# Performance work log

Hardware: AMD Instinct MI355X
Metric: run time of the kernel (lower is better)

## Reference

```python
import jax, jax.numpy as jnp
import numpy as np

# S4D (diagonal state space) layer, version=1, bidirectional.
# Faithful to the standard minimal S4D: ZOH-discretized diagonal kernel via
# Vandermonde, causal FFT convolution, D skip, GELU, then 1x1-conv GLU.


def _s4d(u, log_dt, C_re, C_im, log_A_real, A_imag, D_skip, W_glu, b_glu):
    # u: (B, L, H)
    B, L, Hd = u.shape
    dt = jnp.exp(log_dt)                                   # (H,)
    A = -jnp.exp(log_A_real) + 1j * A_imag                 # (H, N2) complex
    dtA = A * dt[:, None]                                  # (H, N2)
    C = (C_re + 1j * C_im) * (jnp.exp(dtA) - 1.0) / A      # (H, N2)
    V = jnp.exp(dtA[:, :, None] * jnp.arange(L))           # (H, N2, L) Vandermonde
    K = 2.0 * jnp.einsum('hn,hnl->hl', C, V).real          # (H, L) SSM kernel
    uT = jnp.swapaxes(u, 1, 2)                             # (B, H, L)
    n = 2 * L                                              # zero-pad for causal conv
    y = jnp.fft.irfft(jnp.fft.rfft(uT, n=n) * jnp.fft.rfft(K, n=n), n=n)[..., :L]
    y = y + uT * D_skip[:, None]                           # skip connection
    y = jax.nn.gelu(y, approximate=False)                  # torch nn.GELU (exact erf)
    # output_linear: Conv1d(H, 2H, 1) + GLU(dim=-2)
    z = jnp.einsum('oh,bhl->bol', W_glu, y) + b_glu[None, :, None]
    y = z[:, :Hd] * jax.nn.sigmoid(z[:, Hd:])
    return jnp.swapaxes(y, 1, 2)                           # (B, L, H)


def setup_inputs() -> dict:
    key = jax.random.key(0)
    B, L, D, N = 64, 2048, 256, 64
    N2 = N // 2
    kx, kf, kr = jax.random.split(key, 3)

    def make_params(k0):
        ks = jax.random.split(k0, 6)
        log_dt = jax.random.uniform(ks[0], (D,)) * (np.log(0.1) - np.log(0.001)) + np.log(0.001)
        C_re = jax.random.normal(ks[1], (D, N2))
        C_im = jax.random.normal(ks[2], (D, N2))
        log_A_real = jnp.log(0.5 * jnp.ones((D, N2), dtype=jnp.float32))
        A_imag = np.pi * jnp.broadcast_to(jnp.arange(N2, dtype=jnp.float32), (D, N2))
        D_skip = jax.random.normal(ks[3], (D,))
        W_glu = jax.random.normal(ks[4], (2 * D, D)) / np.sqrt(D)
        b_glu = jax.random.normal(ks[5], (2 * D,)) * 0.01
        return log_dt, C_re, C_im, log_A_real, A_imag, D_skip, W_glu, b_glu

    pf = make_params(kf)
    pr = make_params(kr)
    names = ['log_dt', 'C_re', 'C_im', 'log_A_real', 'A_imag', 'D_skip', 'W_glu', 'b_glu']
    inp = {'x': jax.random.normal(kx, (B, L, D), dtype=jnp.float32)}
    for n_, v in zip(names, pf):
        inp[n_] = v
    for n_, v in zip(names, pr):
        inp[n_ + '_rev'] = v
    return inp


def reference(x, log_dt, C_re, C_im, log_A_real, A_imag, D_skip, W_glu, b_glu,
              log_dt_rev, C_re_rev, C_im_rev, log_A_real_rev, A_imag_rev,
              D_skip_rev, W_glu_rev, b_glu_rev):
    y_fwd = _s4d(x, log_dt, C_re, C_im, log_A_real, A_imag, D_skip, W_glu, b_glu)
    y_rev = _s4d(x[:, ::-1], log_dt_rev, C_re_rev, C_im_rev, log_A_real_rev,
                 A_imag_rev, D_skip_rev, W_glu_rev, b_glu_rev)
    return y_fwd + y_rev[:, ::-1]
```

## Files before the change

### kernel.cpp

```cpp
#include <hip/hip_runtime.h>
#include <hip/hip_bf16.h>
#include <math.h>

#define Bb 64
#define Ll 2048
#define Hh 256
#define N2v 32
#define NCH 4
#define CLEN (Ll / NCH)

#define WF_OFF 1024
#define BF_OFF 525312
#define GOLD_OFF 529408
#define A2_OFF 529408
#define AF_OFF 4723712
#define WT_OFF 13112320
#define XT_OFF 13243392
#define S_OFF  80352256
#define GT_OFF 214569984
#define WS_NEED 348787712ull
#define GNEW_OFF XT_OFF

typedef __hip_bfloat16 bf16;
typedef __bf16 bf16x8 __attribute__((ext_vector_type(8)));
typedef float f32x4 __attribute__((ext_vector_type(4)));
typedef _Float16 f16;
typedef _Float16 f16x2 __attribute__((ext_vector_type(2)));
typedef _Float16 f16x4 __attribute__((ext_vector_type(4)));
typedef _Float16 f16x8 __attribute__((ext_vector_type(8)));

__device__ __forceinline__ float b2f(bf16 v) { return __bfloat162float(v); }
__device__ __forceinline__ float ldf(const float* p, int i) { return p[i]; }
__device__ __forceinline__ float ldf(const bf16* p, int i) { return b2f(p[i]); }

__device__ __forceinline__ void gl2lds16(const void* g, void* l) {
  __builtin_amdgcn_global_load_lds((const __attribute__((address_space(1))) void*)g,
                                   (__attribute__((address_space(3))) void*)l, 16, 0, 0);
}

__device__ __forceinline__ f32x4 mfma16(f16x8 a, f16x8 b, f32x4 c) {
  return __builtin_amdgcn_mfma_f32_16x16x32_f16(a, b, c, 0, 0, 0);
}

__device__ __forceinline__ bool input_is_bf16(const void* logA) {
  unsigned u = *(const unsigned*)logA;
  return (u >> 16) == (u & 0xffffu);
}

__global__ void s4d_prep(const void* Wf, const void* bfb, const void* Wr,
                         const void* brb, const void* logA, char* ws) {
  const bool bf = input_is_bf16(logA);
  bf16* wdst = (bf16*)(ws + WF_OFF);
  float* bdst = (float*)(ws + BF_OFF);
  const int i = blockIdx.x * 256 + threadIdx.x;
  if (i < 262144) {
    const int dstR = i >> 8, k = i & 255;
    const int ht = dstR >> 7, c = dstR & 127;
    const int mat = c >> 5, hl = c & 31;
    const int srow = mat * 256 + ht * 32 + hl;
    const void* src = (srow < 512) ? Wf : Wr;
    const int j = ((srow < 512) ? srow : srow - 512) * 256 + k;
    const float v = bf ? b2f(((const bf16*)src)[j]) : ((const float*)src)[j];
    wdst[i] = __float2bfloat16(v);
  } else if (i < 262144 + 1024) {
    const int j = i - 262144;
    const void* src = (j < 512) ? bfb : brb;
    const int k = (j < 512) ? j : j - 512;
    bdst[j] = bf ? b2f(((const bf16*)src)[k]) : ((const float*)src)[k];
  }
}

struct ScanP {
  const void* x;
  const void* prm[2][6];
  char* ws;
};

__global__ __launch_bounds__(64) void s4d_prepA(ScanP p) {
  const int d = blockIdx.x >> 8, h = blockIdx.x & 255;
  const int lane = threadIdx.x;
  __shared__ float Ksh[64];
  char* ws = p.ws;
  const bool bf = input_is_bf16(p.prm[0][3]);
#define LDP(w_, i_) (bf ? b2f(((const bf16*)p.prm[d][w_])[i_]) : ((const float*)p.prm[d][w_])[i_])
  const float dt = expf(LDP(0, h));
  const float dsk = LDP(5, h);
  float Kv = 0.f;
  const float dl = (float)lane;
  for (int n = 0; n < 32; ++n) {
    const int idx = h * 32 + n;
    const float Ar = -expf(LDP(3, idx));
    const float Ai = LDP(4, idx);
    const float th = Ai * dt, rr = Ar * dt;
    const float er = expf(rr);
    const float wr = er * cosf(th), wi = er * sinf(th);
    const float den = 1.f / (Ar * Ar + Ai * Ai);
    const float Er = wr - 1.f, Ei = wi;
    const float qr = (Er * Ar + Ei * Ai) * den, qi = (Ei * Ar - Er * Ai) * den;
    const float CR = LDP(1, idx), CI = LDP(2, idx);
    const float cre = 2.f * (CR * qr - CI * qi), cim = 2.f * (CR * qi + CI * qr);
    const float pe = expf(rr * dl), pang = th * dl;
    Kv += cre * pe * cosf(pang) - cim * pe * sinf(pang);
  }
  Ksh[lane] = Kv;
  if (lane < 32) {
    const int idx = h * 32 + lane;
    const float Ar = -expf(LDP(3, idx));
    const float Ai = LDP(4, idx);
    const float th = Ai * dt, rr = Ar * dt;
    const float e64 = expf(rr * 64.f);
    float2 wt;
    wt.x = e64 * cosf(th * 64.f);
    wt.y = e64 * sinf(th * 64.f);
    ((float2*)(ws + WT_OFF))[(d * 256 + h) * 32 + lane] = wt;
  }
  __syncthreads();
  f16* arow = (f16*)(ws + AF_OFF) + ((size_t)(d * 256 + h) * 64 + lane) * 128;
  for (int j = 0; j < 64; ++j) {
    float v = 0.f;
    if (d == 0) { if (j <= lane) v = Ksh[lane - j]; }
    else        { if (j >= lane) v = Ksh[j - lane]; }
    if (j == lane) v += dsk;
    arow[j] = (f16)v;
  }
  const float pexp = (d == 0) ? (float)(lane + 1) : (float)(64 - lane);
  for (int n = 0; n < 32; ++n) {
    const int idx = h * 32 + n;
    const float Ar = -expf(LDP(3, idx));
    const float Ai = LDP(4, idx);
    const float th = Ai * dt, rr = Ar * dt;
    const float er = expf(rr);
    const float wr = er * cosf(th), wi = er * sinf(th);
    const float den = 1.f / (Ar * Ar + Ai * Ai);
    const float Er = wr - 1.f, Ei = wi;
    const float qr = (Er * Ar + Ei * Ai) * den, qi = (Ei * Ar - Er * Ai) * den;
    const float CR = LDP(1, idx), CI = LDP(2, idx);
    const float cre = 2.f * (CR * qr - CI * qi), cim = 2.f * (CR * qi + CI * qr);
    const float pe = expf(rr * pexp), pang = th * pexp;
    const float pwr = pe * cosf(pang), pwi = pe * sinf(pang);
    arow[64 + 2 * n]     = (f16)(cre * pwr - cim * pwi);
    arow[64 + 2 * n + 1] = (f16)(-(cre * pwi + cim * pwr));
  }
  {
    const int n = lane >> 1, im = lane & 1;
    const int idx = h * 32 + n;
    const float Ar = -expf(LDP(3, idx));
    const float Ai = LDP(4, idx);
    const float th = Ai * dt, rr = Ar * dt;
    f16* a2 = (f16*)(ws + A2_OFF) + ((size_t)h * 128 + d * 64 + lane) * 64;
    for (int i = 0; i < 64; ++i) {
      const float pp = (d == 0) ? (float)(63 - i) : (float)i;
      const float e = expf(rr * pp), ang = th * pp;
      a2[i] = (f16)(im ? e * sinf(ang) : e * cosf(ang));
    }
  }
#undef LDP
}

template <typename T>
__device__ __forceinline__ void t1_body(const T* __restrict__ x, char* ws) {
  __shared__ f16 tile[8][264];
  const int b = blockIdx.x, h0 = blockIdx.y * 8;
  const int t = threadIdx.x;
  f16* xT = (f16*)(ws + XT_OFF);
  const int hh = t & 7, lo = t >> 3;
  const int wh = t >> 5, q = t & 31;
  for (int l0 = 0; l0 < 2048; l0 += 256) {
    __syncthreads();
#pragma unroll
    for (int ps = 0; ps < 8; ++ps) {
      const int l = l0 + ps * 32 + lo;
      tile[hh][ps * 32 + lo] = (f16)ldf(x, (b * 2048 + l) * 256 + h0 + hh);
    }
    __syncthreads();
    f16x8 v = *(const f16x8*)(&tile[wh][q * 8]);
    *(f16x8*)(xT + ((size_t)(h0 + wh) * 64 + b) * 2048 + l0 + q * 8) = v;
  }
}

__global__ __launch_bounds__(256) void s4d_t1(const void* x, const void* logA, char* ws) {
  if (input_is_bf16(logA)) t1_body<bf16>((const bf16*)x, ws);
  else                     t1_body<float>((const float*)x, ws);
}

__global__ __launch_bounds__(256) void s4d_krs(char* __restrict__ ws) {
  __shared__ char lds[34816];
  const int bid = blockIdx.x;
  const int h = bid >> 4, cb = bid & 15;
  const int t = threadIdx.x, lane = t & 63, wave = t >> 6;
  const int lm = lane & 15, lq = lane >> 4;
  const f16* xT = (const f16*)(ws + XT_OFF);
  const char* a2b = ws + A2_OFF + (size_t)h * 128 * 64 * 2;
  const int srow = lane >> 3;
  const int sch = (lane & 7) ^ srow;
#pragma unroll
  for (int j = 0; j < 4; ++j) {
    const int rb = wave * 4 + j;
    const int r = rb * 8 + srow;
    gl2lds16(a2b + r * 128 + sch * 16, lds + rb * 1024);
    const int col = cb * 128 + r;
    const int b_ = col >> 5, c_ = col & 31;
    gl2lds16((const char*)(xT + ((size_t)(h * 64 + b_) * 2048 + c_ * 64)) + sch * 16,
             lds + 16384 + rb * 1024);
  }
  __syncthreads();
  f32x4 acc[2][8];
#pragma unroll
  for (int i = 0; i < 2; ++i)
#pragma unroll
    for (int j = 0; j < 8; ++j) acc[i][j] = (f32x4){0.f, 0.f, 0.f, 0.f};
#pragma unroll
  for (int kb = 0; kb < 2; ++kb) {
    const int cA = kb * 4 + lq;
    f16x8 au[2], a2f[8];
#pragma unroll
    for (int i = 0; i < 2; ++i) {
      const int r = wave * 32 + i * 16 + lm;
      au[i] = *(const f16x8*)(lds + 16384 + r * 128 + ((cA ^ (r & 7)) * 16));
    }
#pragma unroll
    for (int j = 0; j < 8; ++j) {
      const int r = j * 16 + lm;
      a2f[j] = *(const f16x8*)(lds + r * 128 + ((cA ^ (r & 7)) * 16));
    }
#pragma unroll
    for (int i = 0; i < 2; ++i)
#pragma unroll
      for (int j = 0; j < 8; ++j) acc[i][j] = mfma16(au[i], a2f[j], acc[i][j]);
  }
  __syncthreads();
  f16* Cl = (f16*)lds;
#pragma unroll
  for (int i = 0; i < 2; ++i)
#pragma unroll
    for (int j = 0; j < 8; ++j)
#pragma unroll
      for (int r = 0; r < 4; ++r)
        Cl[(wave * 32 + i * 16 + lq * 4 + r) * 136 + j * 16 + lm] = (f16)acc[i][j][r];
  __syncthreads();
  const int n = t & 31, dir = (t >> 5) & 1, bl = wave;
  const float2 wt = ((const float2*)(ws + WT_OFF))[(dir * 256 + h) * 32 + n];
  f16* Sg = (f16*)(ws + S_OFF) + ((size_t)h * 2048 + cb * 128 + bl * 32) * 128 + dir * 64 + 2 * n;
  const f16* Cr = Cl + (size_t)(bl * 32) * 136 + dir * 64 + 2 * n;
  float sr = 0.f, si = 0.f;
  const int c0 = dir ? 31 : 0, cstep = dir ? -1 : 1;
  for (int it = 0; it < 32; ++it) {
    const int c = c0 + it * cstep;
    f16x2 sv; sv[0] = (f16)sr; sv[1] = (f16)si;
    *(f16x2*)(Sg + (size_t)c * 128) = sv;
    const float rr = (float)Cr[c * 136], ri = (float)Cr[c * 136 + 1];
    const float a = sr;
    sr = wt.x * a - wt.y * si + rr;
    si = wt.x * si + wt.y * a + ri;
  }
}

__global__ __launch_bounds__(256) void s4d_k3(char* __restrict__ ws) {
  __shared__ char lds[57344];
  const int bid = blockIdx.x;
  const int h = bid >> 5, cb = bid & 31;
  const int t = threadIdx.x, lane = t & 63, wave = t >> 6;
  const int lm = lane & 15, lq = lane >> 4;
  const f16* xT = (const f16*)(ws + XT_OFF);
  const char* afb = ws + AF_OFF + (size_t)h * 64 * 128 * 2;
  const char* arb = ws + AF_OFF + (size_t)(256 + h) * 64 * 128 * 2;
  const char* sb = ws + S_OFF;
  {
    const int sr4 = lane >> 4, c16 = lane & 15;
#pragma unroll
    for (int j = 0; j < 4; ++j) {
      const int rb = wave * 4 + j;
      const int r = rb * 4 + sr4;
      const int sc = c16 ^ (r & 7);
      gl2lds16(afb + r * 256 + sc * 16, lds + rb * 1024);
      gl2lds16(arb + r * 256 + sc * 16, lds + 16384 + rb * 1024);
    }
  }
  {
    const int sr8 = lane >> 3, c8 = lane & 7;
#pragma unroll
    for (int j = 0; j < 2; ++j) {
      const int rb = wave * 2 + j;
      const int clr = rb * 8 + sr8;
      const int col = cb * 64 + clr;
      const int b_ = col >> 5, c_ = col & 31;
      const int sc = c8 ^ (clr & 7);
      gl2lds16((const char*)(xT + ((size_t)(h * 64 + b_) * 2048 + c_ * 64)) + sc * 16,
               lds + 32768 + rb * 1024);
      const char* srow = sb + ((size_t)h * 2048 + col) * 256;
      gl2lds16(srow + sc * 16,       lds + 40960 + rb * 1024);
      gl2lds16(srow + 128 + sc * 16, lds + 49152 + rb * 1024);
    }
  }
  __syncthreads();
  const int dir = wave >> 1, chf = wave & 1;
  const char* At = lds + dir * 16384;
  f32x4 acc[4][2];
#pragma unroll
  for (int i = 0; i < 4; ++i)
#pragma unroll
    for (int j = 0; j < 2; ++j) acc[i][j] = (f32x4){0.f, 0.f, 0.f, 0.f};
#pragma unroll
  for (int kb = 0; kb < 4; ++kb) {
    f16x8 av[4], bv[2];
    const int cA = kb * 4 + lq;
#pragma unroll
    for (int i = 0; i < 4; ++i) {
      const int r = i * 16 + lm;
      av[i] = *(const f16x8*)(At + r * 256 + ((cA ^ (r & 7)) * 16));
    }
    const char* Bt = lds + 32768 + ((kb < 2) ? 0 : (dir ? 16384 : 8192));
    const int cB = (kb & 1) * 4 + lq;
#pragma unroll
    for (int j = 0; j < 2; ++j) {
      const int r = chf * 32 + j * 16 + lm;
      bv[j] = *(const f16x8*)(Bt + r * 128 + ((cB ^ (r & 7)) * 16));
    }
#pragma unroll
    for (int i = 0; i < 4; ++i)
#pragma unroll
      for (int j = 0; j < 2; ++j) acc[i][j] = mfma16(av[i], bv[j], acc[i][j]);
  }
  f16* gT = (f16*)(ws + GT_OFF);
#pragma unroll
  for (int i = 0; i < 4; ++i)
#pragma unroll
    for (int j = 0; j < 2; ++j) {
      const int col = cb * 64 + chf * 32 + j * 16 + lm;
      const int b_ = col >> 5, c_ = col & 31;
      const int i0 = i * 16 + lq * 4;
      f16x4 o;
#pragma unroll
      for (int r = 0; r < 4; ++r) {
        const float y = acc[i][j][r];
        o[r] = (f16)(0.5f * y * (1.f + erff(y * 0.70710678118654752f)));
      }
      *(f16x4*)(gT + ((size_t)((dir * 256 + h) * 64 + b_)) * 2048 + c_ * 64 + i0) = o;
    }
}

__global__ __launch_bounds__(256) void s4d_tr(char* __restrict__ ws) {
  const int bid = blockIdx.x;
  const int mt = bid & 7, hq = (bid >> 3) & 7, b = (bid >> 6) & 63, dir = bid >> 12;
  const int lane = threadIdx.x & 63, wave = threadIdx.x >> 6;
  const int hb = hq * 32 + wave * 8;
  const f16* gT = (const f16*)(ws + GT_OFF);
  bf16* gm = (bf16*)(ws + GNEW_OFF) + (size_t)dir * (Bb * Ll * Hh);
#pragma unroll
  for (int mp = 0; mp < 4; ++mp) {
    const size_t l = (size_t)mt * 256 + mp * 64 + lane;
    ushort us[8];
#pragma unroll
    for (int e = 0; e < 8; ++e) {
      const float f = (float)gT[((size_t)((dir * 256 + hb + e) * 64 + b)) * 2048 + l];
      bf16 bb = __float2bfloat16(f);
      us[e] = *(ushort*)&bb;
    }
    uint4 o;
    o.x = (unsigned)us[0] | ((unsigned)us[1] << 16);
    o.y = (unsigned)us[2] | ((unsigned)us[3] << 16);
    o.z = (unsigned)us[4] | ((unsigned)us[5] << 16);
    o.w = (unsigned)us[6] | ((unsigned)us[7] << 16);
    *(uint4*)((char*)gm + ((size_t)b * 2048 + l) * 512 + hb * 2) = o;
  }
}

template <typename T>
__device__ __forceinline__ void scan_body(
    const T* __restrict__ x, const T* ldt_p, const T* cre_p, const T* cim_p,
    const T* lar_p, const T* aim_p, const T* dsk_p, bf16* gbase, float2* S) {
  const int t = threadIdx.x;
  const int lane = t & 63;
  const int ch = t >> 6;
  const int hloc = lane & 7;
  const int ngrp = lane >> 3;
  const int b = blockIdx.x;
  const int hblk = blockIdx.y;
  const int dir = blockIdx.z;
  const int h = hblk * 8 + hloc;

  const float dt = expf(ldf(ldt_p, h));
  float wre[4], wim[4], cre[4], cim[4], sre[4], sim[4];
#pragma unroll
  for (int j = 0; j < 4; ++j) {
    const int idx = h * N2v + ngrp * 4 + j;
    const float Ar = -expf(ldf(lar_p, idx));
    const float Ai = ldf(aim_p, idx);
    const float er = expf(Ar * dt);
    const float wr = er * cosf(Ai * dt), wi = er * sinf(Ai * dt);
    wre[j] = wr; wim[j] = wi;
    const float Er = wr - 1.0f, Ei = wi;
    const float den = 1.0f / (Ar * Ar + Ai * Ai);
    const float qr = (Er * Ar + Ei * Ai) * den;
    const float qi = (Ei * Ar - Er * Ai) * den;
    const float CR = ldf(cre_p, idx);
    const float CI = ldf(cim_p, idx);
    cre[j] = 2.0f * (CR * qr - CI * qi);
    cim[j] = 2.0f * (CR * qi + CI * qr);
    sre[j] = 0.0f; sim[j] = 0.0f;
  }
  const float dsk = ldf(dsk_p, h);

  const int base = b * (Ll * Hh) + h;
  const int stride = dir ? -Hh : Hh;
  const T* x0 = x + base + (dir ? (Ll - 1) * Hh : 0);
  bf16* g0 = gbase + dir * (Bb * Ll * Hh) + base + (dir ? (Ll - 1) * Hh : 0);

  if (ch < NCH - 1) {
    const T* xp = x0 + ch * CLEN * stride;
    for (int it = 0; it < CLEN / 4; ++it) {
      const float u0 = ldf(xp, 0);
      const float u1 = ldf(xp, stride);
      const float u2 = ldf(xp, 2 * stride);
      const float u3 = ldf(xp, 3 * stride);
      xp += 4 * stride;
#pragma unroll
      for (int k = 0; k < 4; ++k) {
        const float U = (k == 0) ? u0 : (k == 1) ? u1 : (k == 2) ? u2 : u3;
#pragma unroll
        for (int j = 0; j < 4; ++j) {
          const float a = sre[j], bb = sim[j];
          sre[j] = fmaf(wre[j], a, fmaf(-wim[j], bb, U));
          sim[j] = fmaf(wre[j], bb, wim[j] * a);
        }
      }
    }
#pragma unroll
    for (int j = 0; j < 4; ++j)
      S[((ch * 8 + ngrp) * 4 + j) * 8 + hloc] = (float2){sre[j], sim[j]};
  }
  __syncthreads();

  float pr[4], pi[4];
#pragma unroll
  for (int j = 0; j < 4; ++j) { pr[j] = wre[j]; pi[j] = wim[j]; }
  for (int q = 0; q < 9; ++q) {
#pragma unroll
    for (int j = 0; j < 4; ++j) {
      const float a = pr[j], bb = pi[j];
      pr[j] = fmaf(a, a, -bb * bb);
      pi[j] = 2.0f * a * bb;
    }
  }
#pragma unroll
  for (int j = 0; j < 4; ++j) { sre[j] = 0.0f; sim[j] = 0.0f; }
  for (int cc = 0; cc < ch; ++cc) {
#pragma unroll
    for (int j = 0; j < 4; ++j) {
      const float2 sv = S[((cc * 8 + ngrp) * 4 + j) * 8 + hloc];
      const float a = sre[j], bb = sim[j];
      sre[j] = fmaf(pr[j], a, fmaf(-pi[j], bb, sv.x));
      sim[j] = fmaf(pr[j], bb, fmaf(pi[j], a, sv.y));
    }
  }

  const T* xp = x0 + ch * CLEN * stride;
  bf16* gp = g0 + ch * CLEN * stride;
  const bool q0 = (ngrp & 1) != 0;
  const bool q1 = (ngrp & 2) != 0;
  const bool q2 = (ngrp & 4) != 0;
  for (int it = 0; it < CLEN / 8; ++it) {
    float u[8], P[8];
#pragma unroll
    for (int k = 0; k < 8; ++k) u[k] = ldf(xp, k * stride);
    xp += 8 * stride;
#pragma unroll
    for (int k = 0; k < 8; ++k) {
      float pa = 0.0f, pb = 0.0f;
#pragma unroll
      for (int j = 0; j < 4; ++j) {
        const float a = sre[j], bb = sim[j];
        sre[j] = fmaf(wre[j], a, fmaf(-wim[j], bb, u[k]));
        sim[j] = fmaf(wre[j], bb, wim[j] * a);
        pa = fmaf(cre[j], sre[j], pa);
        pb = fmaf(cim[j], sim[j], pb);
      }
      P[k] = pa - pb;
    }
    const float Q0 = (q0 ? P[1] : P[0]) + __shfl_xor(q0 ? P[0] : P[1], 8);
    const float Q1 = (q0 ? P[3] : P[2]) + __shfl_xor(q0 ? P[2] : P[3], 8);
    const float Q2 = (q0 ? P[5] : P[4]) + __shfl_xor(q0 ? P[4] : P[5], 8);
    const float Q3 = (q0 ? P[7] : P[6]) + __shfl_xor(q0 ? P[6] : P[7], 8);
    const float R0 = (q1 ? Q1 : Q0) + __shfl_xor(q1 ? Q0 : Q1, 16);
    const float R1 = (q1 ? Q3 : Q2) + __shfl_xor(q1 ? Q2 : Q3, 16);
    const float Tt = (q2 ? R1 : R0) + __shfl_xor(q2 ? R0 : R1, 32);
    const float s01 = q0 ? u[1] : u[0];
    const float s23 = q0 ? u[3] : u[2];
    const float s45 = q0 ? u[5] : u[4];
    const float s67 = q0 ? u[7] : u[6];
    const float Uo = q2 ? (q1 ? s67 : s45) : (q1 ? s23 : s01);
    const float y = fmaf(dsk, Uo, Tt);
    const float ge = 0.5f * y * (1.0f + erff(y * 0.70710678118654752f));
    gp[ngrp * stride] = __float2bfloat16(ge);
    gp += 8 * stride;
  }
}

__global__ __launch_bounds__(256) void s4d_scan(ScanP p) {
  __shared__ float2 S[(NCH - 1) * 8 * 4 * 8];
  const int dir = blockIdx.z;
  bf16* g = (bf16*)(p.ws + GOLD_OFF);
  if (input_is_bf16(p.prm[0][3])) {
    scan_body<bf16>((const bf16*)p.x, (const bf16*)p.prm[dir][0],
                    (const bf16*)p.prm[dir][1], (const bf16*)p.prm[dir][2],
                    (const bf16*)p.prm[dir][3], (const bf16*)p.prm[dir][4],
                    (const bf16*)p.prm[dir][5], g, S);
  } else {
    scan_body<float>((const float*)p.x, (const float*)p.prm[dir][0],
                     (const float*)p.prm[dir][1], (const float*)p.prm[dir][2],
                     (const float*)p.prm[dir][3], (const float*)p.prm[dir][4],
                     (const float*)p.prm[dir][5], g, S);
  }
}

__global__ __launch_bounds__(256, 2) void s4d_glu_gemm(const char* __restrict__ ws,
                                                       void* __restrict__ out_v,
                                                       const void* logA,
                                                       unsigned goff) {
  __shared__ char lds[49152];
  const bool obf = input_is_bf16(logA);
  const char* gf = ws + goff;
  const char* gr = gf + (size_t)Bb * Ll * Hh * 2;
  const char* wre = ws + WF_OFF;
  const float* bias = (const float*)(ws + BF_OFF);

  const int lane = threadIdx.x & 63;
  const int wave = threadIdx.x >> 6;
  const int lm = lane & 15;
  const int lq = lane >> 4;
  const int mt = blockIdx.x >> 3;
  const int ht = blockIdx.x & 7;
  const size_t mrow0 = (size_t)mt * 128;

  f32x4 acc[4][4];
#pragma unroll
  for (int i = 0; i < 4; ++i)
#pragma unroll
    for (int ct = 0; ct < 4; ++ct) acc[i][ct] = (f32x4){0.f, 0.f, 0.f, 0.f};

  const int srow = lane >> 3;
  const int sch = (lane & 7) ^ srow;

  for (int ks = 0; ks < 4; ++ks) {
    const int kb_byte = ks * 128;
    __syncthreads();
#pragma unroll
    for (int j = 0; j < 12; ++j) {
      const int s = wave * 12 + j;
      const int tile = s >> 4;
      const int rb = s & 15;
      const int r = rb * 8 + srow;
      const char* gsrc;
      if (tile == 0)      gsrc = gf + (mrow0 + r) * 512 + kb_byte + sch * 16;
      else if (tile == 1) gsrc = gr + (mrow0 + r) * 512 + kb_byte + sch * 16;
      else                gsrc = wre + (size_t)(ht * 128 + r) * 512 + kb_byte + sch * 16;
      gl2lds16(gsrc, lds + tile * 16384 + rb * 1024);
    }
    __syncthreads();
    const char* Ab = lds + ((wave >> 1) ? 16384 : 0);
    const char* Bt = lds + 32768;
#pragma unroll
    for (int kb = 0; kb < 2; ++kb) {
      bf16x8 af[4], bf_[4];
      const int c = kb * 4 + lq;
#pragma unroll
      for (int i = 0; i < 4; ++i) {
        const int r = (wave & 1) * 64 + i * 16 + lm;
        af[i] = *(const bf16x8*)(Ab + r * 128 + ((c ^ (r & 7)) * 16));
      }
#pragma unroll
      for (int ct = 0; ct < 4; ++ct) {
        const int r = (wave >> 1) * 64 + ct * 16 + lm;
        bf_[ct] = *(const bf16x8*)(Bt + r * 128 + ((c ^ (r & 7)) * 16));
      }
#pragma unroll
      for (int i = 0; i < 4; ++i)
#pragma unroll
        for (int ct = 0; ct < 4; ++ct)
          acc[i][ct] = __builtin_amdgcn_mfma_f32_16x16x32_bf16(af[i], bf_[ct], acc[i][ct], 0, 0, 0);
    }
  }

  __syncthreads();
  float* xb = (float*)lds;
  if (wave >= 2) {
#pragma unroll
    for (int ctl = 0; ctl < 2; ++ctl) {
      const float blo = bias[512 + ht * 32 + ctl * 16 + lm];
      const float bhi = bias[768 + ht * 32 + ctl * 16 + lm];
#pragma unroll
      for (int i = 0; i < 4; ++i)
#pragma unroll
        for (int r = 0; r < 4; ++r) {
          const float z3 = acc[i][ctl][r] + blo;
          const float z4 = acc[i][ctl + 2][r] + bhi;
          xb[(((wave & 1) * 2 + ctl) * 16 + i * 4 + r) * 64 + lane] =
              z3 * (1.0f / (1.0f + expf(-z4)));
        }
    }
  }
  __syncthreads();
  if (wave < 2) {
#pragma unroll
    for (int ctl = 0; ctl < 2; ++ctl) {
      const int hout = ht * 32 + ctl * 16 + lm;
      const float blo = bias[hout];
      const float bhi = bias[256 + hout];
#pragma unroll
      for (int i = 0; i < 4; ++i)
#pragma unroll
        for (int r = 0; r < 4; ++r) {
          const float z1 = acc[i][ctl][r] + blo;
          const float z2 = acc[i][ctl + 2][r] + bhi;
          const float v = z1 * (1.0f / (1.0f + expf(-z2))) +
                          xb[(((wave & 1) * 2 + ctl) * 16 + i * 4 + r) * 64 + lane];
          const size_t m = mrow0 + (wave & 1) * 64 + i * 16 + lq * 4 + r;
          if (obf) ((bf16*)out_v)[m * Hh + hout] = __float2bfloat16(v);
          else     ((float*)out_v)[m * Hh + hout] = v;
        }
    }
  }
}

extern "C" void kernel_launch(void* const* d_in, const int* in_sizes, int n_in,
                              void* d_out, int out_size, void* d_ws, size_t ws_size,
                              hipStream_t stream) {
  ScanP p;
  p.x = d_in[0];
  for (int d = 0; d < 2; ++d)
    for (int j = 0; j < 6; ++j) p.prm[d][j] = d_in[1 + d * 8 + j];
  p.ws = (char*)d_ws;

  hipLaunchKernelGGL(s4d_prep, dim3(1028), dim3(256), 0, stream,
                     d_in[7], d_in[8], d_in[15], d_in[16], d_in[4], (char*)d_ws);

  if (ws_size >= (size_t)WS_NEED) {
    hipLaunchKernelGGL(s4d_prepA, dim3(512), dim3(64), 0, stream, p);
    hipLaunchKernelGGL(s4d_t1, dim3(64, 32), dim3(256), 0, stream,
                       d_in[0], d_in[4], (char*)d_ws);
    hipLaunchKernelGGL(s4d_krs, dim3(4096), dim3(256), 0, stream, (char*)d_ws);
    hipLaunchKernelGGL(s4d_k3, dim3(8192), dim3(256), 0, stream, (char*)d_ws);
    hipLaunchKernelGGL(s4d_tr, dim3(8192), dim3(256), 0, stream, (char*)d_ws);
    hipLaunchKernelGGL(s4d_glu_gemm, dim3(8192), dim3(256), 0, stream,
                       (const char*)d_ws, d_out, d_in[4], (unsigned)GNEW_OFF);
  } else {
    hipLaunchKernelGGL(s4d_scan, dim3(Bb, Hh / 8, 2), dim3(256), 0, stream, p);
    hipLaunchKernelGGL(s4d_glu_gemm, dim3(8192), dim3(256), 0, stream,
                       (const char*)d_ws, d_out, d_in[4], (unsigned)GOLD_OFF);
  }
}
```

Baseline: 803.0 us.

## Vectorize input transpose and remap block indices for cache locality across kernels

The transpose kernel now loads the input with 4-wide vector loads into a 64x64 fp32 LDS tile and writes 16 contiguous f16 per thread, instead of scalar loads over 8-channel tiles. This is meant to make global reads wider and better coalesced. The krs, k3 and GLU GEMM kernels get swizzled block-to-tile mappings so that concurrently running blocks share nearby weight and state data in L2. Their launch bounds are raised to ask for more resident blocks, which may force register spills.

```diff
diff --git a/kernel.cpp b/kernel.cpp
--- a/kernel.cpp
+++ b/kernel.cpp
@@ -32,6 +32,15 @@
 __device__ __forceinline__ float b2f(bf16 v) { return __bfloat162float(v); }
 __device__ __forceinline__ float ldf(const float* p, int i) { return p[i]; }
 __device__ __forceinline__ float ldf(const bf16* p, int i) { return b2f(p[i]); }
+
+__device__ __forceinline__ float4 ld4f(const float* p) { return *(const float4*)p; }
+__device__ __forceinline__ float4 ld4f(const bf16* p) {
+  ushort4 u = *(const ushort4*)p;
+  float4 r;
+  r.x = b2f(*(bf16*)&u.x); r.y = b2f(*(bf16*)&u.y);
+  r.z = b2f(*(bf16*)&u.z); r.w = b2f(*(bf16*)&u.w);
+  return r;
+}
 
 __device__ __forceinline__ void gl2lds16(const void* g, void* l) {
   __builtin_amdgcn_global_load_lds((const __attribute__((address_space(1))) void*)g,
@@ -158,35 +167,46 @@
 }
 
 template <typename T>
-__device__ __forceinline__ void t1_body(const T* __restrict__ x, char* ws) {
-  __shared__ f16 tile[8][264];
-  const int b = blockIdx.x, h0 = blockIdx.y * 8;
+__device__ __forceinline__ void t1_body(const T* __restrict__ x, char* ws, float* tile) {
+  const int b = blockIdx.x, h0 = blockIdx.y * 64;
   const int t = threadIdx.x;
   f16* xT = (f16*)(ws + XT_OFF);
-  const int hh = t & 7, lo = t >> 3;
-  const int wh = t >> 5, q = t & 31;
-  for (int l0 = 0; l0 < 2048; l0 += 256) {
+  const int h4r = (t & 15) * 4;
+  const int lrb = t >> 4;
+  const int hw = t & 63;
+  const int lo = t >> 6;
+  const int lbase = blockIdx.z * 512;
+  for (int l0 = lbase; l0 < lbase + 512; l0 += 64) {
     __syncthreads();
 #pragma unroll
-    for (int ps = 0; ps < 8; ++ps) {
-      const int l = l0 + ps * 32 + lo;
-      tile[hh][ps * 32 + lo] = (f16)ldf(x, (b * 2048 + l) * 256 + h0 + hh);
+    for (int p = 0; p < 4; ++p) {
+      const int l = p * 16 + lrb;
+      const float4 v = ld4f(x + ((size_t)b * 2048 + l0 + l) * 256 + h0 + h4r);
+      *(float4*)&tile[l * 68 + h4r] = v;
     }
     __syncthreads();
-    f16x8 v = *(const f16x8*)(&tile[wh][q * 8]);
-    *(f16x8*)(xT + ((size_t)(h0 + wh) * 64 + b) * 2048 + l0 + q * 8) = v;
+    f16x8 o0, o1;
+#pragma unroll
+    for (int j = 0; j < 8; ++j) o0[j] = (f16)tile[(lo * 16 + j) * 68 + hw];
+#pragma unroll
+    for (int j = 0; j < 8; ++j) o1[j] = (f16)tile[(lo * 16 + 8 + j) * 68 + hw];
+    f16* dst = xT + ((size_t)(h0 + hw) * 64 + b) * 2048 + l0 + lo * 16;
+    *(f16x8*)dst = o0;
+    *(f16x8*)(dst + 8) = o1;
   }
 }
 
 __global__ __launch_bounds__(256) void s4d_t1(const void* x, const void* logA, char* ws) {
-  if (input_is_bf16(logA)) t1_body<bf16>((const bf16*)x, ws);
-  else                     t1_body<float>((const float*)x, ws);
-}
-
-__global__ __launch_bounds__(256) void s4d_krs(char* __restrict__ ws) {
+  __shared__ float tile[64 * 68];
+  if (input_is_bf16(logA)) t1_body<bf16>((const bf16*)x, ws, tile);
+  else                     t1_body<float>((const float*)x, ws, tile);
+}
+
+__global__ __launch_bounds__(256, 3) void s4d_krs(char* __restrict__ ws) {
   __shared__ char lds[34816];
   const int bid = blockIdx.x;
-  const int h = bid >> 4, cb = bid & 15;
+  const int h = ((bid >> 7) << 3) | (bid & 7);
+  const int cb = (bid >> 3) & 15;
   const int t = threadIdx.x, lane = t & 63, wave = t >> 6;
   const int lm = lane & 15, lq = lane >> 4;
   const f16* xT = (const f16*)(ws + XT_OFF);
@@ -255,10 +275,11 @@
   }
 }
 
-__global__ __launch_bounds__(256) void s4d_k3(char* __restrict__ ws) {
+__global__ __launch_bounds__(256, 2) void s4d_k3(char* __restrict__ ws) {
   __shared__ char lds[57344];
   const int bid = blockIdx.x;
-  const int h = bid >> 5, cb = bid & 31;
+  const int h = ((bid >> 8) << 3) | (bid & 7);
+  const int cb = (bid >> 3) & 31;
   const int t = threadIdx.x, lane = t & 63, wave = t >> 6;
   const int lm = lane & 15, lq = lane >> 4;
   const f16* xT = (const f16*)(ws + XT_OFF);
@@ -513,7 +534,7 @@
   }
 }
 
-__global__ __launch_bounds__(256, 2) void s4d_glu_gemm(const char* __restrict__ ws,
+__global__ __launch_bounds__(256, 3) void s4d_glu_gemm(const char* __restrict__ ws,
                                                        void* __restrict__ out_v,
                                                        const void* logA,
                                                        unsigned goff) {
@@ -528,8 +549,9 @@
   const int wave = threadIdx.x >> 6;
   const int lm = lane & 15;
   const int lq = lane >> 4;
-  const int mt = blockIdx.x >> 3;
-  const int ht = blockIdx.x & 7;
+  const int bid = blockIdx.x;
+  const int mt = ((bid >> 6) << 3) | (bid & 7);
+  const int ht = (bid >> 3) & 7;
   const size_t mrow0 = (size_t)mt * 128;
 
   f32x4 acc[4][4];
@@ -636,7 +658,7 @@
 
   if (ws_size >= (size_t)WS_NEED) {
     hipLaunchKernelGGL(s4d_prepA, dim3(512), dim3(64), 0, stream, p);
-    hipLaunchKernelGGL(s4d_t1, dim3(64, 32), dim3(256), 0, stream,
+    hipLaunchKernelGGL(s4d_t1, dim3(64, 4, 4), dim3(256), 0, stream,
                        d_in[0], d_in[4], (char*)d_ws);
     hipLaunchKernelGGL(s4d_krs, dim3(4096), dim3(256), 0, stream, (char*)d_ws);
     hipLaunchKernelGGL(s4d_k3, dim3(8192), dim3(256), 0, stream, (char*)d_ws);
```

Measured after the change: 931.8 us. +16.0%, slower.
